# Optimization experiments

Measured on AMD Instinct MI355X. Metric: run time of the kernel, lower is better.

Reference implementation:

```python
import jax, jax.numpy as jnp
import numpy as np

B, P, PD = 32, 196, 768          # batch, n_subdivs, subdiv feature dim
D, H, L, NC = 768, 12, 8, 1000   # n_dims, n_heads, n_blocks, n_classes
HD = D // H                      # per-head dim (64)


def _pos_emb(n_pos, d):
    # faithful to _sinusoidal_positional_embeddings: row i (timestep) parity picks sin/cos
    i = jnp.arange(n_pos, dtype=jnp.float32)[:, None]
    j = jnp.arange(d, dtype=jnp.float32)[None, :]
    sin_v = jnp.sin(i / jnp.power(10000.0, j / d))
    cos_v = jnp.cos(i / jnp.power(10000.0, (j - 1.0) / d))
    return jnp.where((jnp.arange(n_pos)[:, None] % 2) == 0, sin_v, cos_v)  # (n_pos, d)


def _layernorm(x, g, b, eps=1e-5):
    m = jnp.mean(x, axis=-1, keepdims=True)
    v = jnp.var(x, axis=-1, keepdims=True)
    return (x - m) * jax.lax.rsqrt(v + eps) * g + b


def setup_inputs() -> dict:
    key = jax.random.key(0)
    ks = iter(jax.random.split(key, 16))
    nrm = lambda shape, s=0.02: jax.random.normal(next(ks), shape, jnp.float32) * s
    return {
        "x": jax.random.normal(next(ks), (B, P, PD), jnp.float32),
        "W_emb": nrm((PD, D)), "b_emb": jnp.zeros((D,), jnp.float32),
        "v_class": jax.random.uniform(next(ks), (1, D), jnp.float32),
        "ln1_g": jnp.ones((L, D), jnp.float32), "ln1_b": jnp.zeros((L, D), jnp.float32),
        "Wq": nrm((L, H, HD, HD)), "bq": jnp.zeros((L, H, HD), jnp.float32),
        "Wk": nrm((L, H, HD, HD)), "bk": jnp.zeros((L, H, HD), jnp.float32),
        "Wv": nrm((L, H, HD, HD)), "bv": jnp.zeros((L, H, HD), jnp.float32),
        "ln2_g": jnp.ones((L, D), jnp.float32), "ln2_b": jnp.zeros((L, D), jnp.float32),
        "W1": nrm((L, D, 4 * D)), "b1": jnp.zeros((L, 4 * D), jnp.float32),
        "W2": nrm((L, 4 * D, D)), "b2": jnp.zeros((L, D), jnp.float32),
        "W_cls": nrm((D, NC)), "b_cls": jnp.zeros((NC,), jnp.float32),
    }


def reference(x, W_emb, b_emb, v_class, ln1_g, ln1_b, Wq, bq, Wk, bk, Wv, bv,
              ln2_g, ln2_b, W1, b1, W2, b2, W_cls, b_cls):
    b = x.shape[0]
    pos = _pos_emb(P, D)                                  # (P, D), same for every sample
    h = x @ W_emb + b_emb + pos                           # (B, P, D)
    cls_tok = jnp.broadcast_to(v_class[None], (b, 1, D))
    h = jnp.concatenate([cls_tok, h], axis=1)             # (B, S, D), S = P + 1
    S = P + 1
    attns = []
    for l in range(L):
        # --- MHSA: each head reads only its own hd-slice of the input ---
        xn = _layernorm(h, ln1_g[l], ln1_b[l])
        xh = xn.reshape(b, S, H, HD)
        q = jnp.einsum('bshi,hij->bshj', xh, Wq[l]) + bq[l]
        k = jnp.einsum('bshi,hij->bshj', xh, Wk[l]) + bk[l]
        v = jnp.einsum('bshi,hij->bshj', xh, Wv[l]) + bv[l]
        scores = jnp.einsum('bqhj,bkhj->bhqk', q, k) / (HD ** 0.5)
        a = jax.nn.softmax(scores, axis=-1)               # (B, H, S, S)
        attns.append(jnp.mean(a, axis=1))                 # mean over heads, (B, S, S)
        o = jnp.einsum('bhqk,bkhj->bqhj', a, v).reshape(b, S, D)
        h = o + h                                         # residual 1
        # --- MLP ---
        xn2 = _layernorm(h, ln2_g[l], ln2_b[l])
        m = jax.nn.gelu(xn2 @ W1[l] + b1[l], approximate=False)
        h = m @ W2[l] + b2[l] + h                         # residual 2
    cls = h[:, 0]
    pred = jax.nn.softmax(cls @ W_cls + b_cls, axis=-1)   # (B, NC)
    return pred, jnp.stack(attns)                         # attns: (L, B, S, S)
```

## Files before the change

kernel.cpp:

```cpp
#include <hip/hip_runtime.h>
#include <cstdint>

typedef unsigned short u16;
typedef __attribute__((ext_vector_type(8))) short bf16x8;
typedef __attribute__((ext_vector_type(4))) float f32x4;

#define DEV static __device__ __forceinline__

#define BB 32
#define PP 196
#define DD 768
#define HH 12
#define HDD 64
#define SS 197
#define NTOK 6304
#define NTOKX 6272
#define NCLS 1000
#define DD4 3072
#define KPAD 224
#define NBH 384
#define NLAY 8

DEV u16 f2bf(float f){ unsigned u=__float_as_uint(f); u += 0x7FFFu + ((u>>16)&1u); return (u16)(u>>16); }
DEV float bf2f(u16 u){ return __uint_as_float(((unsigned)u)<<16); }

typedef __attribute__((address_space(1))) void gas1;
typedef __attribute__((address_space(3))) void las3;

DEV void gld16(const void* g, void* l){
  __builtin_amdgcn_global_load_lds((gas1*)(uintptr_t)g, (las3*)(unsigned)(uintptr_t)l, 16, 0, 0);
}

struct __align__(8) u16x4 { u16 x,y,z,w; };


__global__ void pos_kernel(float* __restrict__ pos){
  int idx = blockIdx.x*256 + threadIdx.x;
  if (idx >= PP*DD) return;
  int p = idx / DD, j = idx - p*DD;
  int odd = p & 1;
  float e = ((float)j - (float)odd) * (1.0f/(float)DD);
  float arg = (float)p / powf(10000.0f, e);
  pos[idx] = odd ? cosf(arg) : sinf(arg);
}

__global__ void f32_to_bf16_kernel(const float* __restrict__ in, u16* __restrict__ out, int n4){
  int i = blockIdx.x*256 + threadIdx.x;
  if (i >= n4) return;
  float4 v = reinterpret_cast<const float4*>(in)[i];
  u16x4 o = { f2bf(v.x), f2bf(v.y), f2bf(v.z), f2bf(v.w) };
  reinterpret_cast<u16x4*>(out)[i] = o;
}

__global__ void clstok_kernel(const float* __restrict__ vcls, float* __restrict__ h){
  int b = blockIdx.x;
  for (int i = threadIdx.x; i < DD; i += 256)
    h[(size_t)b*SS*DD + i] = vcls[i];
}

__global__ void transpose_kernel(const float* __restrict__ in, u16* __restrict__ out, int R, int C){
  __shared__ float tile[32][33];
  int bx = blockIdx.x*32, by = blockIdx.y*32;
  size_t zoff = (size_t)blockIdx.z * R * C;
  const float* src = in + zoff;
  u16* dst = out + zoff;
  int tx = threadIdx.x, ty = threadIdx.y;
  #pragma unroll
  for (int q=0;q<4;q++)
    tile[ty + q*8][tx] = src[(size_t)(by + ty + q*8)*C + bx + tx];
  __syncthreads();
  #pragma unroll
  for (int q=0;q<4;q++)
    dst[(size_t)(bx + ty + q*8)*R + by + tx] = f2bf(tile[tx][ty + q*8]);
}

__global__ void ln_kernel(const float* __restrict__ h, const float* __restrict__ g,
                          const float* __restrict__ b, u16* __restrict__ xn){
  int t = blockIdx.x*4 + (threadIdx.x>>6);
  int lane = threadIdx.x & 63;
  const float4* src = reinterpret_cast<const float4*>(h + (size_t)t*DD);
  float4 xv[3];
  float s = 0.f, s2 = 0.f;
  #pragma unroll
  for (int p=0;p<3;p++){
    xv[p] = src[p*64 + lane];
    s  += xv[p].x + xv[p].y + xv[p].z + xv[p].w;
    s2 += xv[p].x*xv[p].x + xv[p].y*xv[p].y + xv[p].z*xv[p].z + xv[p].w*xv[p].w;
  }
  #pragma unroll
  for (int o=32;o>0;o>>=1){ s += __shfl_xor(s,o); s2 += __shfl_xor(s2,o); }
  float mean = s * (1.f/(float)DD);
  float rstd = rsqrtf(s2*(1.f/(float)DD) - mean*mean + 1e-5f);
  #pragma unroll
  for (int p=0;p<3;p++){
    int base = p*256 + lane*4;
    u16x4 o4 = { f2bf((xv[p].x-mean)*rstd*g[base+0]+b[base+0]),
                 f2bf((xv[p].y-mean)*rstd*g[base+1]+b[base+1]),
                 f2bf((xv[p].z-mean)*rstd*g[base+2]+b[base+2]),
                 f2bf((xv[p].w-mean)*rstd*g[base+3]+b[base+3]) };
    *reinterpret_cast<u16x4*>(&xn[(size_t)t*DD + base]) = o4;
  }
}

template<int EPI>
__global__ __launch_bounds__(256) void gemm_bf16(
    const u16* __restrict__ A, const u16* __restrict__ BT, int M, int K,
    const float* __restrict__ bias, const float* __restrict__ pos,
    float* __restrict__ Hout, u16* __restrict__ Bout)
{
  __shared__ __align__(16) u16 As[64*32];
  __shared__ __align__(16) u16 Bs[128*32];
  const int tid = threadIdx.x;
  const int wave = tid>>6, lane = tid&63;
  const int bm = blockIdx.x, bn = blockIdx.y;
  const int wr = wave>>1, wc = wave&1;

  f32x4 acc[2][4] = {};

  const int lr = lane>>2;
  const int lc = (lane&3)*8;
  int ar = bm*64 + wave*16 + lr; if (ar > M-1) ar = M-1;
  const u16* aS  = A  + (size_t)ar*K + lc;
  const u16* bS0 = BT + (size_t)(bn*128 + wave*32 +      lr)*K + lc;
  const u16* bS1 = BT + (size_t)(bn*128 + wave*32 + 16 + lr)*K + lc;
  u16* aD  = &As[wave*512];
  u16* bD0 = &Bs[wave*1024];
  u16* bD1 = &Bs[wave*1024 + 512];

  for (int kt = 0; kt < K; kt += 32) {
    if (kt) __syncthreads();
    gld16(aS  + kt, aD);
    gld16(bS0 + kt, bD0);
    gld16(bS1 + kt, bD1);
    __syncthreads();
    bf16x8 af[2], bfv[4];
    #pragma unroll
    for (int i=0;i<2;i++)
      af[i] = *reinterpret_cast<const bf16x8*>(&As[(wr*32 + i*16 + (lane&15))*32 + (lane>>4)*8]);
    #pragma unroll
    for (int j=0;j<4;j++)
      bfv[j] = *reinterpret_cast<const bf16x8*>(&Bs[(wc*64 + j*16 + (lane&15))*32 + (lane>>4)*8]);
    #pragma unroll
    for (int i=0;i<2;i++)
      #pragma unroll
      for (int j=0;j<4;j++)
        acc[i][j] = __builtin_amdgcn_mfma_f32_16x16x32_bf16(af[i], bfv[j], acc[i][j], 0, 0, 0);
  }

  const int rowb = bm*64 + wr*32 + (lane>>4)*4;
  const int colb = bn*128 + wc*64 + (lane&15);
  const int Nst = gridDim.y * 128;
  #pragma unroll
  for (int i=0;i<2;i++){
    #pragma unroll
    for (int j=0;j<4;j++){
      int col = colb + j*16;
      #pragma unroll
      for (int r=0;r<4;r++){
        int row = rowb + i*16 + r;
        if (row >= M) continue;
        float v = acc[i][j][r];
        if (EPI == 0){
          int bb = row / PP, p = row - bb*PP;
          Hout[((size_t)(bb*SS + 1 + p))*DD + col] = v + bias[col] + pos[p*DD + col];
        } else if (EPI == 1){
          float xg = v + bias[col];
          Bout[(size_t)row*Nst + col] = f2bf(0.5f*xg*(1.f + erff(xg*0.7071067811865475f)));
        } else {
          Hout[(size_t)row*DD + col] += v + bias[col];
        }
      }
    }
  }
}

__global__ __launch_bounds__(256) void qkv_kernel(
    const u16* __restrict__ xn,
    const u16* __restrict__ WqT, const u16* __restrict__ WkT, const u16* __restrict__ WvT,
    const float* __restrict__ bq, const float* __restrict__ bk, const float* __restrict__ bv,
    u16* __restrict__ qb, u16* __restrict__ kb, u16* __restrict__ vb)
{
  const int LDA = 72;
  __shared__ __align__(16) u16 Asm[128*72];
  __shared__ __align__(16) u16 Wsm[3][64*72];
  const int tid = threadIdx.x, wave = tid>>6, lane = tid&63;
  const int bm = blockIdx.x, hd = blockIdx.y;

  #pragma unroll
  for (int ps=0; ps<4; ++ps){
    int e = (ps*256 + tid)*8;
    int row = e>>6, col = e&63;
    int gr = bm*128 + row; if (gr > NTOK-1) gr = NTOK-1;
    *reinterpret_cast<int4*>(&Asm[row*LDA + col]) =
        *reinterpret_cast<const int4*>(&xn[(size_t)gr*DD + hd*HDD + col]);
  }
  const u16* wsrc[3] = { WqT + hd*4096, WkT + hd*4096, WvT + hd*4096 };
  #pragma unroll
  for (int w=0; w<3; ++w)
    #pragma unroll
    for (int ps=0; ps<2; ++ps){
      int e = (ps*256 + tid)*8;
      int row = e>>6, col = e&63;
      *reinterpret_cast<int4*>(&Wsm[w][row*LDA + col]) =
          *reinterpret_cast<const int4*>(&wsrc[w][row*64 + col]);
    }
  __syncthreads();

  bf16x8 af[2][2];
  #pragma unroll
  for (int i=0;i<2;i++)
    #pragma unroll
    for (int kk=0;kk<2;kk++)
      af[i][kk] = *reinterpret_cast<const bf16x8*>(&Asm[(wave*32 + i*16 + (lane&15))*LDA + kk*32 + (lane>>4)*8]);

  f32x4 acc[3][2][4] = {};
  #pragma unroll
  for (int w=0;w<3;w++)
    #pragma unroll
    for (int kk=0;kk<2;kk++)
      #pragma unroll
      for (int j=0;j<4;j++){
        bf16x8 bfv = *reinterpret_cast<const bf16x8*>(&Wsm[w][(j*16 + (lane&15))*LDA + kk*32 + (lane>>4)*8]);
        #pragma unroll
        for (int i=0;i<2;i++)
          acc[w][i][j] = __builtin_amdgcn_mfma_f32_16x16x32_bf16(af[i][kk], bfv, acc[w][i][j], 0,0,0);
      }

  const float* bqh = bq + hd*HDD;
  const float* bkh = bk + hd*HDD;
  const float* bvh = bv + hd*HDD;
  #pragma unroll
  for (int i=0;i<2;i++)
    #pragma unroll
    for (int j=0;j<4;j++){
      int d = j*16 + (lane&15);
      #pragma unroll
      for (int r=0;r<4;r++){
        int t = bm*128 + wave*32 + i*16 + (lane>>4)*4 + r;
        if (t >= NTOK) continue;
        int b = t / SS, sx = t - b*SS;
        size_t bh = (size_t)b*HH + hd;
        qb[(bh*SS + sx)*HDD + d] = f2bf(acc[0][i][j][r] + bqh[d]);
        kb[(bh*SS + sx)*HDD + d] = f2bf(acc[1][i][j][r] + bkh[d]);
        vb[(bh*KPAD + sx)*HDD + d] = f2bf(acc[2][i][j][r] + bvh[d]);
      }
    }
}

__global__ __launch_bounds__(256) void scores_kernel(
    const u16* __restrict__ qb, const u16* __restrict__ kb, u16* __restrict__ sc)
{
  const int LDA = 72;
  __shared__ __align__(16) u16 Qs[128*72];
  __shared__ __align__(16) u16 Ks[128*72];
  const int tid = threadIdx.x, wave = tid>>6, lane = tid&63;
  const int bm = blockIdx.x, bn = blockIdx.y, bh = blockIdx.z;
  #pragma unroll
  for (int ps=0; ps<4; ++ps){
    int e = (ps*256 + tid)*8;
    int row = e>>6, col = e&63;
    int qr = bm*128 + row; if (qr > SS-1) qr = SS-1;
    int kr = bn*128 + row; if (kr > SS-1) kr = SS-1;
    *reinterpret_cast<int4*>(&Qs[row*LDA + col]) = *reinterpret_cast<const int4*>(&qb[((size_t)bh*SS + qr)*HDD + col]);
    *reinterpret_cast<int4*>(&Ks[row*LDA + col]) = *reinterpret_cast<const int4*>(&kb[((size_t)bh*SS + kr)*HDD + col]);
  }
  __syncthreads();
  const int wr = wave>>1, wc = wave&1;
  f32x4 acc[4][4] = {};
  #pragma unroll
  for (int kk=0;kk<2;kk++){
    bf16x8 af[4], bfv[4];
    #pragma unroll
    for (int i=0;i<4;i++) af[i] = *reinterpret_cast<const bf16x8*>(&Qs[(wr*64+i*16+(lane&15))*LDA + kk*32 + (lane>>4)*8]);
    #pragma unroll
    for (int j=0;j<4;j++) bfv[j] = *reinterpret_cast<const bf16x8*>(&Ks[(wc*64+j*16+(lane&15))*LDA + kk*32 + (lane>>4)*8]);
    #pragma unroll
    for (int i=0;i<4;i++)
      #pragma unroll
      for (int j=0;j<4;j++)
        acc[i][j] = __builtin_amdgcn_mfma_f32_16x16x32_bf16(af[i], bfv[j], acc[i][j], 0,0,0);
  }
  #pragma unroll
  for (int i=0;i<4;i++)
    #pragma unroll
    for (int j=0;j<4;j++){
      int kg = bn*128 + wc*64 + j*16 + (lane&15);
      #pragma unroll
      for (int r=0;r<4;r++){
        int qg = bm*128 + wr*64 + i*16 + (lane>>4)*4 + r;
        if (qg < SS && kg < SS)
          sc[((size_t)bh*SS + qg)*KPAD + kg] = f2bf(acc[i][j][r] * 0.125f);
      }
    }
}

__global__ void softmax_kernel(u16* __restrict__ sc){
  int row = blockIdx.x*4 + (threadIdx.x>>6);
  int lane = threadIdx.x & 63;
  u16* src = sc + (size_t)row*KPAD;
  float v[4]; float mx = -1e30f;
  #pragma unroll
  for (int p=0;p<4;p++){
    int c = lane + p*64;
    v[p] = (c < SS) ? bf2f(src[c]) : -1e30f;
    mx = fmaxf(mx, v[p]);
  }
  #pragma unroll
  for (int o=32;o>0;o>>=1) mx = fmaxf(mx, __shfl_xor(mx,o));
  float s = 0.f;
  #pragma unroll
  for (int p=0;p<4;p++){
    int c = lane + p*64;
    v[p] = (c < SS) ? expf(v[p]-mx) : 0.f;
    s += v[p];
  }
  #pragma unroll
  for (int o=32;o>0;o>>=1) s += __shfl_xor(s,o);
  float inv = 1.f / s;
  #pragma unroll
  for (int p=0;p<4;p++){
    int c = lane + p*64;
    if (c < KPAD) src[c] = f2bf((c < SS) ? v[p]*inv : 0.f);
  }
}

__global__ void attnmean_kernel(const u16* __restrict__ attn, float* __restrict__ outp){
  int qi = blockIdx.x, b = blockIdx.y, kk = threadIdx.x;
  if (kk >= SS) return;
  float s = 0.f;
  #pragma unroll
  for (int h=0; h<HH; ++h)
    s += bf2f(attn[(((size_t)b*HH + h)*SS + qi)*KPAD + kk]);
  outp[((size_t)b*SS + qi)*SS + kk] = s * (1.f/12.f);
}

__global__ __launch_bounds__(256) void av_kernel(
    const u16* __restrict__ attn, const u16* __restrict__ vb, float* __restrict__ h)
{
  const int LDA = 40;
  const int LDB = 40;
  __shared__ __align__(16) u16 Asm[128*40];
  __shared__ __align__(16) u16 Bsm[64*40];
  const int tid = threadIdx.x, wave = tid>>6, lane = tid&63;
  const int bm = blockIdx.x, bh = blockIdx.y;
  const int b = bh / HH, hd = bh - b*HH;
  f32x4 acc[2][4] = {};
  for (int k0 = 0; k0 < KPAD; k0 += 32){
    if (k0) __syncthreads();
    #pragma unroll
    for (int ps=0; ps<2; ++ps){
      int e = (ps*256 + tid)*8;
      int row = e>>5, col = e&31;
      int ar = bm*128 + row; if (ar > SS-1) ar = SS-1;
      *reinterpret_cast<int4*>(&Asm[row*LDA + col]) =
          *reinterpret_cast<const int4*>(&attn[((size_t)bh*SS + ar)*KPAD + k0 + col]);
    }
    {
      int kk = tid>>3;
      int d0 = (tid&7)*8;
      bf16x8 vv = *reinterpret_cast<const bf16x8*>(&vb[((size_t)bh*KPAD + k0 + kk)*HDD + d0]);
      #pragma unroll
      for (int q=0;q<8;q++) Bsm[(d0+q)*LDB + kk] = (u16)vv[q];
    }
    __syncthreads();
    bf16x8 af[2], bfv[4];
    #pragma unroll
    for (int i=0;i<2;i++) af[i] = *reinterpret_cast<const bf16x8*>(&Asm[(wave*32 + i*16 + (lane&15))*LDA + (lane>>4)*8]);
    #pragma unroll
    for (int j=0;j<4;j++) bfv[j] = *reinterpret_cast<const bf16x8*>(&Bsm[(j*16 + (lane&15))*LDB + (lane>>4)*8]);
    #pragma unroll
    for (int i=0;i<2;i++)
      #pragma unroll
      for (int j=0;j<4;j++)
        acc[i][j] = __builtin_amdgcn_mfma_f32_16x16x32_bf16(af[i], bfv[j], acc[i][j], 0,0,0);
  }
  #pragma unroll
  for (int i=0;i<2;i++)
    #pragma unroll
    for (int j=0;j<4;j++){
      int d = j*16 + (lane&15);
      #pragma unroll
      for (int r=0;r<4;r++){
        int sx = bm*128 + wave*32 + i*16 + (lane>>4)*4 + r;
        if (sx < SS)
          h[((size_t)b*SS + sx)*DD + hd*HDD + d] += acc[i][j][r];
      }
    }
}

__global__ __launch_bounds__(256) void logits_kernel(
    const float* __restrict__ h, const float* __restrict__ Wc,
    const float* __restrict__ bc, float* __restrict__ logits)
{
  __shared__ float xs[DD];
  const int b = blockIdx.x, tid = threadIdx.x;
  for (int i = tid; i < DD; i += 256) xs[i] = h[(size_t)b*SS*DD + i];
  __syncthreads();
  const int c = blockIdx.y*250 + tid;
  if (tid >= 250 || c >= NCLS) return;
  float acc = bc[c];
  const float* wcol = Wc + c;
  #pragma unroll 16
  for (int k = 0; k < DD; ++k)
    acc += xs[k] * wcol[(size_t)k*NCLS];
  logits[(size_t)b*NCLS + c] = acc;
}

__global__ __launch_bounds__(256) void pred_softmax_kernel(
    const float* __restrict__ logits, float* __restrict__ outp)
{
  __shared__ float red[256];
  const int b = blockIdx.x, tid = threadIdx.x;
  float acc[4], mx = -1e30f;
  #pragma unroll
  for (int m=0;m<4;m++){
    int c = tid + m*256;
    acc[m] = (c < NCLS) ? logits[(size_t)b*NCLS + c] : -1e30f;
    mx = fmaxf(mx, acc[m]);
  }
  red[tid] = mx; __syncthreads();
  for (int o=128;o>0;o>>=1){ if (tid<o) red[tid] = fmaxf(red[tid], red[tid+o]); __syncthreads(); }
  mx = red[0]; __syncthreads();
  float ex[4]; float s = 0.f;
  #pragma unroll
  for (int m=0;m<4;m++){
    int c = tid + m*256;
    ex[m] = (c < NCLS) ? expf(acc[m]-mx) : 0.f;
    s += ex[m];
  }
  red[tid] = s; __syncthreads();
  for (int o=128;o>0;o>>=1){ if (tid<o) red[tid] += red[tid+o]; __syncthreads(); }
  float inv = 1.f / red[0];
  #pragma unroll
  for (int m=0;m<4;m++){
    int c = tid + m*256;
    if (c < NCLS) outp[(size_t)b*NCLS + c] = ex[m]*inv;
  }
}

extern "C" void kernel_launch(void* const* d_in, const int* in_sizes, int n_in,
                              void* d_out, int out_size, void* d_ws, size_t ws_size,
                              hipStream_t stream)
{
  const float* x      = (const float*)d_in[0];
  const float* W_emb  = (const float*)d_in[1];
  const float* b_emb  = (const float*)d_in[2];
  const float* v_class= (const float*)d_in[3];
  const float* ln1_g  = (const float*)d_in[4];
  const float* ln1_b  = (const float*)d_in[5];
  const float* Wq     = (const float*)d_in[6];
  const float* bq     = (const float*)d_in[7];
  const float* Wk     = (const float*)d_in[8];
  const float* bk     = (const float*)d_in[9];
  const float* Wv     = (const float*)d_in[10];
  const float* bv     = (const float*)d_in[11];
  const float* ln2_g  = (const float*)d_in[12];
  const float* ln2_b  = (const float*)d_in[13];
  const float* W1     = (const float*)d_in[14];
  const float* b1     = (const float*)d_in[15];
  const float* W2     = (const float*)d_in[16];
  const float* b2     = (const float*)d_in[17];
  const float* W_cls  = (const float*)d_in[18];
  const float* b_cls  = (const float*)d_in[19];
  (void)in_sizes; (void)n_in; (void)out_size;
  float* outp = (float*)d_out;

  char* ws = (char*)d_ws;
  size_t off = 0;
  auto alloc = [&](size_t bytes)->char*{
    char* p = ws + off;
    off = (off + bytes + 255) & ~((size_t)255);
    return p;
  };
  float* pos   = (float*)alloc((size_t)PP*DD*4);
  float* hbuf  = (float*)alloc((size_t)NTOK*DD*4);
  u16*   xnb   = (u16*)  alloc((size_t)NTOK*DD*2);
  u16*   WembT = (u16*)  alloc((size_t)DD*DD*2);
  u16*   W1Tl  = (u16*)  alloc((size_t)DD*DD4*2);
  u16*   W2Tl  = (u16*)  alloc((size_t)DD*DD4*2);
  u16*   WqT   = (u16*)  alloc((size_t)NLAY*HH*HDD*HDD*2);
  u16*   WkT   = (u16*)  alloc((size_t)NLAY*HH*HDD*HDD*2);
  u16*   WvT   = (u16*)  alloc((size_t)NLAY*HH*HDD*HDD*2);
  u16*   qbuf  = (u16*)  alloc((size_t)NBH*SS*HDD*2);
  u16*   kbuf  = (u16*)  alloc((size_t)NBH*SS*HDD*2);
  u16*   vbuf  = (u16*)  alloc((size_t)NBH*KPAD*HDD*2);
  u16*   scb   = (u16*)  alloc((size_t)NBH*SS*KPAD*2);
  float* logitsb = (float*)alloc((size_t)BB*NCLS*4);
  u16*   mbuf  = qbuf;
  u16*   xbf   = scb;
  if (ws_size < off) return;

  hipMemsetAsync(vbuf, 0, (size_t)NBH*KPAD*HDD*2, stream);
  pos_kernel<<<(PP*DD+255)/256, 256, 0, stream>>>(pos);
  f32_to_bf16_kernel<<<(NTOKX*DD/4+255)/256, 256, 0, stream>>>(x, xbf, NTOKX*DD/4);
  dim3 tb(32,8);
  transpose_kernel<<<dim3(DD/32, DD/32, 1), tb, 0, stream>>>(W_emb, WembT, DD, DD);
  transpose_kernel<<<dim3(2,2,NLAY*HH), tb, 0, stream>>>(Wq, WqT, HDD, HDD);
  transpose_kernel<<<dim3(2,2,NLAY*HH), tb, 0, stream>>>(Wk, WkT, HDD, HDD);
  transpose_kernel<<<dim3(2,2,NLAY*HH), tb, 0, stream>>>(Wv, WvT, HDD, HDD);

  gemm_bf16<0><<<dim3(98, 6), 256, 0, stream>>>(xbf, WembT, NTOKX, DD, b_emb, pos, hbuf, nullptr);
  clstok_kernel<<<BB, 256, 0, stream>>>(v_class, hbuf);

  for (int l=0; l<NLAY; ++l){
    ln_kernel<<<NTOK/4, 256, 0, stream>>>(hbuf, ln1_g + l*DD, ln1_b + l*DD, xnb);
    qkv_kernel<<<dim3(50, HH), 256, 0, stream>>>(xnb,
        WqT + (size_t)l*HH*4096, WkT + (size_t)l*HH*4096, WvT + (size_t)l*HH*4096,
        bq + l*HH*HDD, bk + l*HH*HDD, bv + l*HH*HDD, qbuf, kbuf, vbuf);
    scores_kernel<<<dim3(2,2,NBH), 256, 0, stream>>>(qbuf, kbuf, scb);
    softmax_kernel<<<NBH*SS/4, 256, 0, stream>>>(scb);
    attnmean_kernel<<<dim3(SS, BB), 256, 0, stream>>>(scb, outp + 32000 + (size_t)l*BB*SS*SS);
    av_kernel<<<dim3(2, NBH), 256, 0, stream>>>(scb, vbuf, hbuf);
    ln_kernel<<<NTOK/4, 256, 0, stream>>>(hbuf, ln2_g + l*DD, ln2_b + l*DD, xnb);
    transpose_kernel<<<dim3(DD4/32, DD/32, 1), tb, 0, stream>>>(W1 + (size_t)l*DD*DD4, W1Tl, DD, DD4);
    gemm_bf16<1><<<dim3(99, 24), 256, 0, stream>>>(xnb, W1Tl, NTOK, DD, b1 + l*DD4, nullptr, nullptr, mbuf);
    transpose_kernel<<<dim3(DD/32, DD4/32, 1), tb, 0, stream>>>(W2 + (size_t)l*DD*DD4, W2Tl, DD4, DD);
    gemm_bf16<2><<<dim3(99, 6), 256, 0, stream>>>(mbuf, W2Tl, NTOK, DD4, b2 + l*DD, nullptr, hbuf, nullptr);
  }
  logits_kernel<<<dim3(BB, 4), 256, 0, stream>>>(hbuf, W_cls, b_cls, logitsb);
  pred_softmax_kernel<<<BB, 256, 0, stream>>>(logitsb, outp);
}
```

Measured before the change: 2.086 ms.

## Remap GEMM workgroups per XCD and batch MLP weight transposes upfront

The GEMM now uses a 1-D grid and remaps workgroup IDs so that consecutive tiles land on the same XCD chiplet, which improves L2 reuse of the A/B tiles on MI355X's multi-XCD layout. W1 and W2 are transposed for all layers in two launches before the layer loop, replacing 16 per-layer transpose launches. The workspace is reorganised so the MLP hidden buffer aliases the q/k/v/score region, making room for the full per-layer transposed weights. This costs more workspace and adds a little index arithmetic per block.

```diff
diff --git a/kernel.cpp b/kernel.cpp
--- a/kernel.cpp
+++ b/kernel.cpp
@@ -105,6 +105,7 @@
 template<int EPI>
 __global__ __launch_bounds__(256) void gemm_bf16(
     const u16* __restrict__ A, const u16* __restrict__ BT, int M, int K,
+    int nbm, int nbn,
     const float* __restrict__ bias, const float* __restrict__ pos,
     float* __restrict__ Hout, u16* __restrict__ Bout)
 {
@@ -112,7 +113,14 @@
   __shared__ __align__(16) u16 Bs[128*32];
   const int tid = threadIdx.x;
   const int wave = tid>>6, lane = tid&63;
-  const int bm = blockIdx.x, bn = blockIdx.y;
+
+  const int nwg = nbm*nbn;
+  const int wg = blockIdx.x;
+  const int xcd = wg & 7, ii = wg >> 3;
+  const int q8 = nwg >> 3, r8 = nwg & 7;
+  const int lin = (xcd < r8 ? xcd*(q8+1) : r8*(q8+1) + (xcd-r8)*q8) + ii;
+  const int bm = lin / nbn, bn = lin - bm*nbn;
+
   const int wr = wave>>1, wc = wave&1;
 
   f32x4 acc[2][4] = {};
@@ -149,7 +157,7 @@
 
   const int rowb = bm*64 + wr*32 + (lane>>4)*4;
   const int colb = bn*128 + wc*64 + (lane&15);
-  const int Nst = gridDim.y * 128;
+  const int Nst = nbn * 128;
   #pragma unroll
   for (int i=0;i<2;i++){
     #pragma unroll
@@ -472,22 +480,23 @@
     off = (off + bytes + 255) & ~((size_t)255);
     return p;
   };
-  float* pos   = (float*)alloc((size_t)PP*DD*4);
-  float* hbuf  = (float*)alloc((size_t)NTOK*DD*4);
-  u16*   xnb   = (u16*)  alloc((size_t)NTOK*DD*2);
-  u16*   WembT = (u16*)  alloc((size_t)DD*DD*2);
-  u16*   W1Tl  = (u16*)  alloc((size_t)DD*DD4*2);
-  u16*   W2Tl  = (u16*)  alloc((size_t)DD*DD4*2);
-  u16*   WqT   = (u16*)  alloc((size_t)NLAY*HH*HDD*HDD*2);
-  u16*   WkT   = (u16*)  alloc((size_t)NLAY*HH*HDD*HDD*2);
-  u16*   WvT   = (u16*)  alloc((size_t)NLAY*HH*HDD*HDD*2);
-  u16*   qbuf  = (u16*)  alloc((size_t)NBH*SS*HDD*2);
-  u16*   kbuf  = (u16*)  alloc((size_t)NBH*SS*HDD*2);
-  u16*   vbuf  = (u16*)  alloc((size_t)NBH*KPAD*HDD*2);
-  u16*   scb   = (u16*)  alloc((size_t)NBH*SS*KPAD*2);
-  float* logitsb = (float*)alloc((size_t)BB*NCLS*4);
-  u16*   mbuf  = qbuf;
-  u16*   xbf   = scb;
+  float* pos    = (float*)alloc((size_t)PP*DD*4);
+  float* hbuf   = (float*)alloc((size_t)NTOK*DD*4);
+  u16*   xnb    = (u16*)  alloc((size_t)NTOK*DD*2);
+  u16*   WembT  = (u16*)  alloc((size_t)DD*DD*2);
+  u16*   W1Tall = (u16*)  alloc((size_t)NLAY*DD*DD4*2);
+  u16*   W2Tall = (u16*)  alloc((size_t)NLAY*DD*DD4*2);
+  u16*   WqT    = (u16*)  alloc((size_t)NLAY*HH*HDD*HDD*2);
+  u16*   WkT    = (u16*)  alloc((size_t)NLAY*HH*HDD*HDD*2);
+  u16*   WvT    = (u16*)  alloc((size_t)NLAY*HH*HDD*HDD*2);
+  char*  blob   = alloc((size_t)NTOK*DD4*2);
+  float* logitsb= (float*)alloc((size_t)BB*NCLS*4);
+  u16* qbuf = (u16*)blob;
+  u16* kbuf = qbuf + (size_t)NBH*SS*HDD;
+  u16* vbuf = kbuf + (size_t)NBH*SS*HDD;
+  u16* scb  = vbuf + (size_t)NBH*KPAD*HDD;
+  u16* mbuf = (u16*)blob;
+  u16* xbf  = scb;
   if (ws_size < off) return;
 
   hipMemsetAsync(vbuf, 0, (size_t)NBH*KPAD*HDD*2, stream);
@@ -498,8 +507,10 @@
   transpose_kernel<<<dim3(2,2,NLAY*HH), tb, 0, stream>>>(Wq, WqT, HDD, HDD);
   transpose_kernel<<<dim3(2,2,NLAY*HH), tb, 0, stream>>>(Wk, WkT, HDD, HDD);
   transpose_kernel<<<dim3(2,2,NLAY*HH), tb, 0, stream>>>(Wv, WvT, HDD, HDD);
-
-  gemm_bf16<0><<<dim3(98, 6), 256, 0, stream>>>(xbf, WembT, NTOKX, DD, b_emb, pos, hbuf, nullptr);
+  transpose_kernel<<<dim3(DD4/32, DD/32, NLAY), tb, 0, stream>>>(W1, W1Tall, DD, DD4);
+  transpose_kernel<<<dim3(DD/32, DD4/32, NLAY), tb, 0, stream>>>(W2, W2Tall, DD4, DD);
+
+  gemm_bf16<0><<<98*6, 256, 0, stream>>>(xbf, WembT, NTOKX, DD, 98, 6, b_emb, pos, hbuf, nullptr);
   clstok_kernel<<<BB, 256, 0, stream>>>(v_class, hbuf);
 
   for (int l=0; l<NLAY; ++l){
@@ -512,10 +523,10 @@
     attnmean_kernel<<<dim3(SS, BB), 256, 0, stream>>>(scb, outp + 32000 + (size_t)l*BB*SS*SS);
     av_kernel<<<dim3(2, NBH), 256, 0, stream>>>(scb, vbuf, hbuf);
     ln_kernel<<<NTOK/4, 256, 0, stream>>>(hbuf, ln2_g + l*DD, ln2_b + l*DD, xnb);
-    transpose_kernel<<<dim3(DD4/32, DD/32, 1), tb, 0, stream>>>(W1 + (size_t)l*DD*DD4, W1Tl, DD, DD4);
-    gemm_bf16<1><<<dim3(99, 24), 256, 0, stream>>>(xnb, W1Tl, NTOK, DD, b1 + l*DD4, nullptr, nullptr, mbuf);
-    transpose_kernel<<<dim3(DD/32, DD4/32, 1), tb, 0, stream>>>(W2 + (size_t)l*DD*DD4, W2Tl, DD4, DD);
-    gemm_bf16<2><<<dim3(99, 6), 256, 0, stream>>>(mbuf, W2Tl, NTOK, DD4, b2 + l*DD, nullptr, hbuf, nullptr);
+    gemm_bf16<1><<<99*24, 256, 0, stream>>>(xnb, W1Tall + (size_t)l*DD*DD4, NTOK, DD, 99, 24,
+                                            b1 + l*DD4, nullptr, nullptr, mbuf);
+    gemm_bf16<2><<<99*6, 256, 0, stream>>>(mbuf, W2Tall + (size_t)l*DD*DD4, NTOK, DD4, 99, 6,
+                                           b2 + l*DD, nullptr, hbuf, nullptr);
   }
   logits_kernel<<<dim3(BB, 4), 256, 0, stream>>>(hbuf, W_cls, b_cls, logitsb);
   pred_softmax_kernel<<<BB, 256, 0, stream>>>(logitsb, outp);
```

Result: faster. 1.954 ms (-6.3%).
